# Optimization experiments

Measured on AMD Instinct MI355X. Metric: run time of the kernel, lower is better.

The kernel has to match this reference:

```python
import jax, jax.numpy as jnp
import numpy as np

# Config constants from the module
E = 64    # n_routed_experts
K = 6     # num_experts_per_tok
D = 128   # hidden_size
M = 80    # moe_intermediate_size
MS = 160  # shared expert intermediate = moe_intermediate_size * n_shared_experts
B, S = 64, 256

def _init_w(k, shape, fan_in):
    # kaiming_uniform(a=sqrt(5)) used by nn.Linear / MoEGate: bound = 1/sqrt(fan_in)
    bound = 1.0 / np.sqrt(fan_in)
    return jax.random.uniform(k, shape, jnp.float32, -bound, bound)

def setup_inputs() -> dict:
    key = jax.random.key(0)
    ks = jax.random.split(key, 8)
    return {
        "hidden_states": jax.random.normal(ks[0], (B, S, D), jnp.float32),
        "gate_w": _init_w(ks[1], (E, D), D),        # MoEGate.linear.weight [E, gating_dim]
        "wg": _init_w(ks[2], (E, D, M), D),          # stacked expert gate_proj (transposed)
        "wu": _init_w(ks[3], (E, D, M), D),          # stacked expert up_proj
        "wd": _init_w(ks[4], (E, M, D), M),          # stacked expert down_proj
        "swg": _init_w(ks[5], (D, MS), D),           # shared expert gate_proj
        "swu": _init_w(ks[6], (D, MS), D),           # shared expert up_proj
        "swd": _init_w(ks[7], (MS, D), MS),          # shared expert down_proj
    }

def reference(hidden_states, gate_w, wg, wu, wd, swg, swu, swd):
    orig_shape = hidden_states.shape
    x = hidden_states.reshape(-1, D)                       # [T, D] flat tokens
    T = x.shape[0]
    # --- MoEGate ('all_agent' mode): softmax scoring + top-k + renorm ---
    scores = jax.nn.softmax(x @ gate_w.T, axis=-1)          # [T, E]
    topk_w, topk_idx = jax.lax.top_k(scores, K)             # [T, K]
    topk_w = topk_w / (jnp.sum(topk_w, axis=-1, keepdims=True) + 1e-20)
    # Scatter top-k weights into dense per-expert combine weights [T, E]
    cw = jnp.zeros_like(scores).at[jnp.arange(T)[:, None], topk_idx].add(topk_w)
    # --- Routed experts: SiLU-gated MLP per expert, combined by cw ---
    g = jax.nn.silu(jnp.einsum('td,edm->tem', x, wg)) * jnp.einsum('td,edm->tem', x, wu)
    y = jnp.einsum('tem,emd,te->td', g, wd, cw)             # down-proj + weighted combine
    # --- Shared experts ---
    shared = (jax.nn.silu(x @ swg) * (x @ swu)) @ swd       # [T, D]
    return (y + shared).reshape(orig_shape)
```

## Files before the change

### kernel.cpp

```cpp
#include <hip/hip_runtime.h>
#include <hip/hip_bf16.h>
#include <math.h>


typedef unsigned short ushort_t;
typedef __attribute__((ext_vector_type(8))) short bf16x8;
typedef __attribute__((ext_vector_type(4))) float f32x4;

#define EALL  66

#define OFF_TOPKI 16384
#define OFF_WORK  409600
#define OFF_TOPKW 802816
#define OFF_PERM  1196032
#define OFF_PERMW 1589248
#define OFF_POS2  1982464
#define OFF_YPERM 2375680
#define OFF_YSH   27541504
#define OFF_WGT   31735808
#define OFF_WUT   33087488
#define OFF_WDP   34439168
#define OFF_XB    36061184
#define OFF_HIST  40255488
#define OFF_BOFF  40321024
#define NEED_FAST 40386560
#define FOFF_YBUF 2375680
#define FOFF_WGT  10764288
#define FOFF_WUT  12115968
#define FOFF_WDP  13467648
#define FOFF_XB   15089664
#define FOFF_HIST 19283968
#define FOFF_BOFF 19349504

__device__ __forceinline__ float bf2f(ushort_t u) {
    unsigned int x = ((unsigned int)u) << 16;
    float f; __builtin_memcpy(&f, &x, 4); return f;
}
__device__ __forceinline__ ushort_t f2bf(float f) {
    unsigned int x; __builtin_memcpy(&x, &f, 4);
    unsigned int r = (x + 0x7fffu + ((x >> 16) & 1u)) >> 16;
    return (ushort_t)r;
}
__device__ __forceinline__ float ldin(const void* p, int i, int f32m) {
    return f32m ? ((const float*)p)[i] : bf2f(((const ushort_t*)p)[i]);
}
__device__ __forceinline__ int detect_f32m(const ushort_t* gw) {
    int lane = threadIdx.x & 63;
    int cnt = 0;
    #pragma unroll
    for (int j = 0; j < 4; ++j) {
        ushort_t u = gw[lane * 4 + j];
        if (((u >> 7) & 0xFF) >= 0x7C) cnt++;
    }
    #pragma unroll
    for (int off = 32; off; off >>= 1) cnt += __shfl_xor(cnt, off);
    return (cnt >= 8) ? 1 : 0;
}
__device__ __forceinline__ void gl16(void* l, const void* g) {
    __builtin_amdgcn_global_load_lds(
        (const __attribute__((address_space(1))) void*)g,
        (__attribute__((address_space(3))) void*)l, 16, 0, 0);
}

__global__ __launch_bounds__(1024) void k_pg(const void* x, const void* gw,
        const void* wg, const void* wu, const void* wd,
        const void* swg, const void* swu, const void* swd,
        ushort_t* wgT, ushort_t* wuT, ushort_t* wdP,
        ushort_t* xB, int* topk_i, float* topk_w, int* histPart) {
    __shared__ __align__(16) char smem[41984];
    int tid = threadIdx.x, bid = blockIdx.x;
    int f32m = detect_f32m((const ushort_t*)gw);

    if (bid < 3 * EALL) {
        float* lds = (float*)smem;
        int mat = bid / EALL, e = bid % EALL;
        if (mat < 2) {
            const void* src  = (mat == 0) ? wg  : wu;
            const void* ssrc = (mat == 0) ? swg : swu;
            for (int i = tid; i < 10240; i += 1024) {
                int d = i / 80, m = i % 80;
                float v = (e < 64) ? ldin(src, e * 10240 + i, f32m)
                                   : ldin(ssrc, d * 160 + (e - 64) * 80 + m, f32m);
                lds[d * 81 + m] = v;
            }
            __syncthreads();
            ushort_t* dst = ((mat == 0) ? wgT : wuT) + e * 10240;
            for (int o = tid; o < 10240; o += 1024) {
                int m = o >> 7, d = o & 127;
                dst[o] = f2bf(lds[d * 81 + m]);
            }
        } else {
            for (int i = tid; i < 10240; i += 1024) {
                float v = (e < 64) ? ldin(wd, e * 10240 + i, f32m)
                                   : ldin(swd, (e - 64) * 10240 + i, f32m);
                int m = i >> 7, d = i & 127;
                lds[m * 129 + d] = v;
            }
            __syncthreads();
            ushort_t* dst = wdP + e * 12288;
            for (int o = tid; o < 12288; o += 1024) {
                int d = o / 96, m = o % 96;
                dst[o] = (m < 80) ? f2bf(lds[m * 129 + d]) : (ushort_t)0;
            }
        }
        return;
    }

    float* gwl  = (float*)smem;
    float (*xl)[128] = (float(*)[128])(smem + 33280);
    int*   histL = (int*)(smem + 41472);
    int b = bid - 3 * EALL;
    for (int i = tid; i < 8192; i += 1024)
        gwl[(i >> 7) * 130 + (i & 127)] = ldin(gw, i, f32m);
    if (tid < 64) histL[tid] = 0;
    __syncthreads();
    int wv = tid >> 6, lane = tid & 63;
    for (int q = 0; q < 4; ++q) {
        int t = b * 64 + wv * 4 + q;
        float xv0, xv1;
        if (f32m) {
            float2 v = ((const float2*)((const float*)x + t * 128))[lane];
            xv0 = v.x; xv1 = v.y;
        } else {
            unsigned int pr = *(const unsigned int*)((const ushort_t*)x + t * 128 + lane * 2);
            xv0 = bf2f((ushort_t)(pr & 0xffffu));
            xv1 = bf2f((ushort_t)(pr >> 16));
        }
        float2 xw; xw.x = xv0; xw.y = xv1;
        *(float2*)&xl[wv][lane * 2] = xw;
        unsigned int packed = (unsigned int)f2bf(xv0) | ((unsigned int)f2bf(xv1) << 16);
        *(unsigned int*)(xB + t * 128 + lane * 2) = packed;
        float acc = 0.f;
        #pragma unroll
        for (int d2 = 0; d2 < 64; ++d2) {
            float2 xv = *(const float2*)&xl[wv][d2 * 2];
            float2 gv = *(const float2*)&gwl[lane * 130 + d2 * 2];
            acc = fmaf(xv.x, gv.x, acc);
            acc = fmaf(xv.y, gv.y, acc);
        }
        float mx = acc;
        #pragma unroll
        for (int off = 32; off; off >>= 1) mx = fmaxf(mx, __shfl_xor(mx, off));
        float p = expf(acc - mx);
        float sm = p;
        #pragma unroll
        for (int off = 32; off; off >>= 1) sm += __shfl_xor(sm, off);
        float sc = p / sm;
        float cur = sc;
        float wk6[6]; int ik[6];
        #pragma unroll
        for (int k = 0; k < 6; ++k) {
            float bv = cur; int bi = lane;
            #pragma unroll
            for (int off = 1; off < 64; off <<= 1) {
                float ov = __shfl_xor(bv, off); int oi = __shfl_xor(bi, off);
                if (ov > bv || (ov == bv && oi < bi)) { bv = ov; bi = oi; }
            }
            wk6[k] = bv; ik[k] = bi;
            if (lane == bi) cur = -INFINITY;
        }
        if (lane == 0) {
            float den = wk6[0] + wk6[1] + wk6[2] + wk6[3] + wk6[4] + wk6[5] + 1e-20f;
            #pragma unroll
            for (int k = 0; k < 6; ++k) {
                topk_i[t * 6 + k] = ik[k];
                topk_w[t * 6 + k] = wk6[k] / den;
                atomicAdd(&histL[ik[k]], 1);
            }
        }
    }
    __syncthreads();
    if (tid < 64) histPart[tid * 256 + b] = histL[tid];
}

__global__ __launch_bounds__(256) void k_scan(int* Wi, const int* histPart,
        int* boffG, int* wk) {
    __shared__ int hl[16384];
    __shared__ int cntL[64], exclL[64], chxL[65];
    int tid = threadIdx.x, lane = tid & 63, wv = tid >> 6;
    for (int j = tid; j < 16384; j += 256) hl[j] = histPart[j];
    __syncthreads();
    for (int ei = 0; ei < 16; ++ei) {
        int e = wv * 16 + ei;
        int carry = 0;
        for (int r = 0; r < 4; ++r) {
            int v = hl[e * 256 + r * 64 + lane];
            int incl = v;
            #pragma unroll
            for (int off = 1; off < 64; off <<= 1) {
                int ts = __shfl_up(incl, off);
                if (lane >= off) incl += ts;
            }
            hl[e * 256 + r * 64 + lane] = carry + incl - v;
            carry += __shfl(incl, 63);
        }
        if (lane == 0) cntL[e] = carry;
    }
    __syncthreads();
    if (tid == 0) {
        int s = 0, cs = 0;
        for (int e = 0; e < 64; ++e) {
            exclL[e] = s; s += cntL[e];
            chxL[e] = cs; cs += (cntL[e] + 127) >> 7;
        }
        chxL[64] = cs;
        Wi[128] = s;
        Wi[193] = cs + 256;
    }
    __syncthreads();
    if (tid < 64) { Wi[tid] = cntL[tid]; Wi[64 + tid] = exclL[tid]; }
    for (int j = tid; j < 16384; j += 256) boffG[j] = hl[j] + exclL[j >> 8];
    wk[tid] = (64 << 16) | tid;
    if (tid < 64) {
        int e = tid, nc = (cntL[e] + 127) >> 7, bb = chxL[e];
        for (int c = 0; c < nc; ++c) wk[256 + bb + c] = (e << 16) | c;
    }
}

__global__ __launch_bounds__(256) void k_scatter(const int* topk_i, const float* topk_w,
        const int* boffG, int* perm, float* permw, int* pos2) {
    __shared__ int lcur[64];
    int tid = threadIdx.x, b = blockIdx.x;
    if (tid < 64) lcur[tid] = boffG[tid * 256 + b];
    __syncthreads();
    for (int i = tid; i < 384; i += 256) {
        int g = b * 384 + i;
        int e = topk_i[g];
        float w = topk_w[g];
        int p = atomicAdd(&lcur[e], 1);
        perm[p]  = b * 64 + i / 6;
        permw[p] = w;
        pos2[g]  = p;
    }
}

template<int FAST>
__global__ __launch_bounds__(256) void k_expert(const ushort_t* x, const ushort_t* wgT,
        const ushort_t* wuT, const ushort_t* wdP, const int* Wi, const int* wk,
        const int* perm, const float* permw, ushort_t* yperm, ushort_t* ysh, float* ybuf) {
    __shared__ __align__(16) char hl[32768];
    __shared__ __align__(16) char bufA[20480];
    __shared__ __align__(16) char bufB[20480];

    if (blockIdx.x >= Wi[193]) return;
    int entry = wk[blockIdx.x];
    int e = entry >> 16, c = entry & 0xffff;
    int tid = threadIdx.x, lid = tid & 63, wv = tid >> 6;
    int kg  = (lid >> 4) * 16;
    int kq8 = (lid >> 4) * 8;

    if (e < 64) {
        int n = Wi[e], base = Wi[64 + e];
        int nrows = n - c * 128; if (nrows > 128) nrows = 128;

        {
            const ushort_t* gS = wgT + e * 10240;
            const ushort_t* uS = wuT + e * 10240;
            #pragma unroll
            for (int i = 0; i < 5; ++i) {
                int s = wv * 320 + i * 64 + lid;
                int row = s >> 4, sc = (s & 15) ^ (row & 7);
                gl16(bufA + wv * 5120 + i * 1024, gS + row * 128 + sc * 8);
                gl16(bufB + wv * 5120 + i * 1024, uS + row * 128 + sc * 8);
            }
        }
        bf16x8 a[2][4];
        #pragma unroll
        for (int tr = 0; tr < 2; ++tr) {
            int arow = wv * 32 + tr * 16 + (lid & 15);
            int r = (arow < nrows) ? arow : (nrows - 1);
            int t = perm[base + c * 128 + r];
            #pragma unroll
            for (int k = 0; k < 4; ++k)
                a[tr][k] = *(const bf16x8*)(x + t * 128 + k * 32 + kq8);
        }
        __syncthreads();

        #pragma unroll
        for (int mi = 0; mi < 5; ++mi) {
            int brow = mi * 16 + (lid & 15);
            int bro = brow * 256, bsw = (brow & 7) << 4;
            f32x4 ag[2], au[2];
            #pragma unroll
            for (int tr = 0; tr < 2; ++tr) {
                ag[tr] = (f32x4){0.f, 0.f, 0.f, 0.f};
                au[tr] = (f32x4){0.f, 0.f, 0.f, 0.f};
            }
            #pragma unroll
            for (int k = 0; k < 4; ++k) {
                int bo = bro + (((k * 64) + kg) ^ bsw);
                bf16x8 bg = *(const bf16x8*)(bufA + bo);
                bf16x8 bu = *(const bf16x8*)(bufB + bo);
                #pragma unroll
                for (int tr = 0; tr < 2; ++tr) {
                    ag[tr] = __builtin_amdgcn_mfma_f32_16x16x32_bf16(a[tr][k], bg, ag[tr], 0, 0, 0);
                    au[tr] = __builtin_amdgcn_mfma_f32_16x16x32_bf16(a[tr][k], bu, au[tr], 0, 0, 0);
                }
            }
            #pragma unroll
            for (int tr = 0; tr < 2; ++tr) {
                #pragma unroll
                for (int rg = 0; rg < 4; ++rg) {
                    float g = ag[tr][rg], uu2 = au[tr][rg];
                    float h = (g / (1.f + __expf(-g))) * uu2;
                    int row = wv * 32 + tr * 16 + (lid >> 4) * 4 + rg;
                    int cb = (mi * 16 + (lid & 15)) * 2;
                    *(ushort_t*)(hl + row * 256 + (cb ^ ((row & 7) << 4))) = f2bf(h);
                }
            }
        }
        {
            int r = wv * 32 + (lid >> 1), ch = 10 + (lid & 1);
            uint4 z = {0u, 0u, 0u, 0u};
            *(uint4*)(hl + r * 256 + ((ch * 16) ^ ((r & 7) << 4))) = z;
        }
        __syncthreads();

        {
            const ushort_t* dS = wdP + e * 12288;
            #pragma unroll
            for (int i = 0; i < 4; ++i) {
                int s = wv * 256 + i * 64 + lid;
                int r = s >> 4, sc = (s & 15) ^ (r & 7);
                int off = (sc < 12) ? sc * 8 : 0;
                gl16(bufA + wv * 4096 + i * 1024, dS + r * 96 + off);
                gl16(bufB + wv * 4096 + i * 1024, dS + (64 + r) * 96 + off);
            }
        }
        __syncthreads();

        bf16x8 bfr[2][3];
        #pragma unroll
        for (int tf = 0; tf < 2; ++tf) {
            int brow = wv * 32 + tf * 16 + (lid & 15);
            #pragma unroll
            for (int k = 0; k < 3; ++k)
                bfr[tf][k] = *(const bf16x8*)(hl + brow * 256 + (((k * 64) + kg) ^ ((brow & 7) << 4)));
        }
        f32x4 acc[8][2];
        #pragma unroll
        for (int dt = 0; dt < 8; ++dt) {
            acc[dt][0] = (f32x4){0.f, 0.f, 0.f, 0.f};
            acc[dt][1] = (f32x4){0.f, 0.f, 0.f, 0.f};
        }
        #pragma unroll
        for (int dt = 0; dt < 8; ++dt) {
            int r = (dt & 3) * 16 + (lid & 15);
            const char* wb = (dt < 4) ? bufA : bufB;
            bf16x8 ad[3];
            #pragma unroll
            for (int k = 0; k < 3; ++k)
                ad[k] = *(const bf16x8*)(wb + r * 256 + (((k * 64) + kg) ^ ((r & 7) << 4)));
            #pragma unroll
            for (int tf = 0; tf < 2; ++tf) {
                f32x4 cc = acc[dt][tf];
                #pragma unroll
                for (int k = 0; k < 3; ++k)
                    cc = __builtin_amdgcn_mfma_f32_16x16x32_bf16(ad[k], bfr[tf][k], cc, 0, 0, 0);
                acc[dt][tf] = cc;
            }
        }

        #pragma unroll
        for (int tf = 0; tf < 2; ++tf) {
            int rloc = wv * 32 + tf * 16 + (lid & 15);
            int rc = (rloc < nrows) ? rloc : (nrows - 1);
            float w = FAST ? permw[base + c * 128 + rc] : 0.f;
            #pragma unroll
            for (int dt = 0; dt < 8; ++dt) {
                if (FAST) {
                    int cb = (dt * 16 + (lid >> 4) * 4) * 2;
                    ushort_t o[4];
                    #pragma unroll
                    for (int rg = 0; rg < 4; ++rg) o[rg] = f2bf(acc[dt][tf][rg] * w);
                    *(uint2*)(hl + rloc * 256 + (cb ^ ((rloc & 7) << 4))) = *(const uint2*)o;
                } else {
                    if (rloc < nrows) {
                        int t = perm[base + c * 128 + rloc];
                        float w2 = permw[base + c * 128 + rloc];
                        int d0 = dt * 16 + (lid >> 4) * 4;
                        #pragma unroll
                        for (int rg = 0; rg < 4; ++rg)
                            atomicAdd(&ybuf[t * 128 + d0 + rg], acc[dt][tf][rg] * w2);
                    }
                }
            }
        }
        if (FAST) {
            #pragma unroll
            for (int ps = 0; ps < 8; ++ps) {
                int row = wv * 32 + ps * 4 + (lid >> 4);
                int cb = (lid & 15) * 16;
                uint4 v = *(const uint4*)(hl + row * 256 + (cb ^ ((row & 7) << 4)));
                if (row < nrows)
                    *(uint4*)(yperm + (size_t)(base + c * 128 + row) * 128 + (lid & 15) * 8) = v;
            }
        }
    } else {
        bf16x8 a1[4];
        int arow = wv * 16 + (lid & 15);
        int t0 = c * 64 + arow;
        #pragma unroll
        for (int k = 0; k < 4; ++k)
            a1[k] = *(const bf16x8*)(x + t0 * 128 + k * 32 + kq8);

        f32x4 acc[8];
        #pragma unroll
        for (int dt = 0; dt < 8; ++dt) acc[dt] = (f32x4){0.f, 0.f, 0.f, 0.f};

        for (int sub = 0; sub < 2; ++sub) {
            int ee = 64 + sub;
            {
                const ushort_t* gS = wgT + ee * 10240;
                const ushort_t* uS = wuT + ee * 10240;
                #pragma unroll
                for (int i = 0; i < 5; ++i) {
                    int s = wv * 320 + i * 64 + lid;
                    int row = s >> 4, sc = (s & 15) ^ (row & 7);
                    gl16(bufA + wv * 5120 + i * 1024, gS + row * 128 + sc * 8);
                    gl16(bufB + wv * 5120 + i * 1024, uS + row * 128 + sc * 8);
                }
            }
            __syncthreads();
            #pragma unroll
            for (int mi = 0; mi < 5; ++mi) {
                int brow = mi * 16 + (lid & 15);
                int bro = brow * 256, bsw = (brow & 7) << 4;
                f32x4 ag = {0.f, 0.f, 0.f, 0.f};
                f32x4 au = {0.f, 0.f, 0.f, 0.f};
                #pragma unroll
                for (int k = 0; k < 4; ++k) {
                    int bo = bro + (((k * 64) + kg) ^ bsw);
                    bf16x8 bg = *(const bf16x8*)(bufA + bo);
                    bf16x8 bu = *(const bf16x8*)(bufB + bo);
                    ag = __builtin_amdgcn_mfma_f32_16x16x32_bf16(a1[k], bg, ag, 0, 0, 0);
                    au = __builtin_amdgcn_mfma_f32_16x16x32_bf16(a1[k], bu, au, 0, 0, 0);
                }
                #pragma unroll
                for (int rg = 0; rg < 4; ++rg) {
                    float g = ag[rg], uu2 = au[rg];
                    float h = (g / (1.f + __expf(-g))) * uu2;
                    int row = wv * 16 + (lid >> 4) * 4 + rg;
                    int cb = (mi * 16 + (lid & 15)) * 2;
                    *(ushort_t*)(hl + row * 256 + (cb ^ ((row & 7) << 4))) = f2bf(h);
                }
            }
            if (sub == 0 && lid < 32) {
                int r = wv * 16 + (lid >> 1), ch = 10 + (lid & 1);
                uint4 z = {0u, 0u, 0u, 0u};
                *(uint4*)(hl + r * 256 + ((ch * 16) ^ ((r & 7) << 4))) = z;
            }
            __syncthreads();
            {
                const ushort_t* dS = wdP + ee * 12288;
                #pragma unroll
                for (int i = 0; i < 4; ++i) {
                    int s = wv * 256 + i * 64 + lid;
                    int r = s >> 4, sc = (s & 15) ^ (r & 7);
                    int off = (sc < 12) ? sc * 8 : 0;
                    gl16(bufA + wv * 4096 + i * 1024, dS + r * 96 + off);
                    gl16(bufB + wv * 4096 + i * 1024, dS + (64 + r) * 96 + off);
                }
            }
            __syncthreads();
            int brow = wv * 16 + (lid & 15);
            #pragma unroll
            for (int dt = 0; dt < 8; ++dt) {
                int r = (dt & 3) * 16 + (lid & 15);
                const char* wb = (dt < 4) ? bufA : bufB;
                bf16x8 ad[3];
                #pragma unroll
                for (int k = 0; k < 3; ++k)
                    ad[k] = *(const bf16x8*)(wb + r * 256 + (((k * 64) + kg) ^ ((r & 7) << 4)));
                f32x4 cc = acc[dt];
                #pragma unroll
                for (int k = 0; k < 3; ++k) {
                    bf16x8 b = *(const bf16x8*)(hl + brow * 256 + (((k * 64) + kg) ^ ((brow & 7) << 4)));
                    cc = __builtin_amdgcn_mfma_f32_16x16x32_bf16(ad[k], b, cc, 0, 0, 0);
                }
                acc[dt] = cc;
            }
            __syncthreads();
        }

        int rloc = wv * 16 + (lid & 15);
        if (FAST) {
            #pragma unroll
            for (int dt = 0; dt < 8; ++dt) {
                int cb = (dt * 16 + (lid >> 4) * 4) * 2;
                ushort_t o[4];
                #pragma unroll
                for (int rg = 0; rg < 4; ++rg) o[rg] = f2bf(acc[dt][rg]);
                *(uint2*)(hl + rloc * 256 + (cb ^ ((rloc & 7) << 4))) = *(const uint2*)o;
            }
            #pragma unroll
            for (int ps = 0; ps < 4; ++ps) {
                int row = wv * 16 + ps * 4 + (lid >> 4);
                int cb = (lid & 15) * 16;
                uint4 v = *(const uint4*)(hl + row * 256 + (cb ^ ((row & 7) << 4)));
                *(uint4*)(ysh + (size_t)(c * 64 + row) * 128 + (lid & 15) * 8) = v;
            }
        } else {
            int t = c * 64 + rloc;
            #pragma unroll
            for (int dt = 0; dt < 8; ++dt) {
                int d0 = dt * 16 + (lid >> 4) * 4;
                #pragma unroll
                for (int rg = 0; rg < 4; ++rg)
                    atomicAdd(&ybuf[t * 128 + d0 + rg], acc[dt][rg]);
            }
        }
    }
}

__global__ __launch_bounds__(256) void k_final_gather(const ushort_t* yperm,
        const ushort_t* ysh, const int* pos2, void* out, const ushort_t* gwDet) {
    int idx = blockIdx.x * 256 + threadIdx.x;
    int t = idx >> 4, cg = (idx & 15) * 8;
    int f32m = detect_f32m(gwDet);
    float acc[8];
    {
        uint4 v = *(const uint4*)(ysh + (size_t)t * 128 + cg);
        const ushort_t* u = (const ushort_t*)&v;
        #pragma unroll
        for (int j = 0; j < 8; ++j) acc[j] = bf2f(u[j]);
    }
    const int* pp = pos2 + t * 6;
    #pragma unroll
    for (int k = 0; k < 6; ++k) {
        int p = pp[k];
        uint4 v = *(const uint4*)(yperm + (size_t)p * 128 + cg);
        const ushort_t* u = (const ushort_t*)&v;
        #pragma unroll
        for (int j = 0; j < 8; ++j) acc[j] += bf2f(u[j]);
    }
    if (f32m) {
        float4 o0 = {acc[0], acc[1], acc[2], acc[3]};
        float4 o1 = {acc[4], acc[5], acc[6], acc[7]};
        float* op = (float*)out + (size_t)t * 128 + cg;
        *(float4*)op = o0; *(float4*)(op + 4) = o1;
    } else {
        ushort_t o[8];
        #pragma unroll
        for (int j = 0; j < 8; ++j) o[j] = f2bf(acc[j]);
        *(uint4*)((ushort_t*)out + (size_t)t * 128 + cg) = *(const uint4*)o;
    }
}

__global__ __launch_bounds__(256) void k_final_ybuf(const float* ybuf, void* out,
        const ushort_t* gwDet) {
    int i = blockIdx.x * 256 + threadIdx.x;
    int f32m = detect_f32m(gwDet);
    float4 v = ((const float4*)ybuf)[i];
    if (f32m) {
        ((float4*)out)[i] = v;
    } else {
        ushort4 o;
        o.x = f2bf(v.x); o.y = f2bf(v.y); o.z = f2bf(v.z); o.w = f2bf(v.w);
        ((ushort4*)out)[i] = o;
    }
}

extern "C" void kernel_launch(void* const* d_in, const int* in_sizes, int n_in,
                              void* d_out, int out_size, void* d_ws, size_t ws_size,
                              hipStream_t stream) {
    (void)in_sizes; (void)n_in; (void)out_size;
    const void* x   = d_in[0];
    const void* gw  = d_in[1];
    const void* wg  = d_in[2];
    const void* wu  = d_in[3];
    const void* wd  = d_in[4];
    const void* swg = d_in[5];
    const void* swu = d_in[6];
    const void* swd = d_in[7];

    char* ws = (char*)d_ws;
    int fast = (ws_size >= (size_t)NEED_FAST) ? 1 : 0;

    int*      Wi     = (int*)d_ws;
    int*      topk_i = (int*)(ws + OFF_TOPKI);
    int*      wklist = (int*)(ws + OFF_WORK);
    float*    topk_w = (float*)(ws + OFF_TOPKW);
    int*      perm   = (int*)(ws + OFF_PERM);
    float*    permw  = (float*)(ws + OFF_PERMW);
    int*      pos2   = (int*)(ws + OFF_POS2);

    ushort_t* yperm = (ushort_t*)(ws + OFF_YPERM);
    ushort_t* ysh   = (ushort_t*)(ws + OFF_YSH);
    float*    ybuf  = (float*)(ws + FOFF_YBUF);
    ushort_t* wgT   = (ushort_t*)(ws + (fast ? OFF_WGT  : FOFF_WGT));
    ushort_t* wuT   = (ushort_t*)(ws + (fast ? OFF_WUT  : FOFF_WUT));
    ushort_t* wdP   = (ushort_t*)(ws + (fast ? OFF_WDP  : FOFF_WDP));
    ushort_t* xB    = (ushort_t*)(ws + (fast ? OFF_XB   : FOFF_XB));
    int*      histP = (int*)(ws + (fast ? OFF_HIST : FOFF_HIST));
    int*      boffG = (int*)(ws + (fast ? OFF_BOFF : FOFF_BOFF));

    if (!fast) hipMemsetAsync(ybuf, 0, 16384 * 128 * 4, stream);

    k_pg<<<3 * EALL + 256, 1024, 0, stream>>>(x, gw, wg, wu, wd, swg, swu, swd,
                                              wgT, wuT, wdP, xB, topk_i, topk_w, histP);
    k_scan<<<1, 256, 0, stream>>>(Wi, histP, boffG, wklist);
    k_scatter<<<256, 256, 0, stream>>>(topk_i, topk_w, boffG, perm, permw, pos2);
    if (fast) {
        k_expert<1><<<1088, 256, 0, stream>>>(xB, wgT, wuT, wdP, Wi, wklist, perm, permw, yperm, ysh, ybuf);
        k_final_gather<<<1024, 256, 0, stream>>>(yperm, ysh, pos2, d_out, (const ushort_t*)gw);
    } else {
        k_expert<0><<<1088, 256, 0, stream>>>(xB, wgT, wuT, wdP, Wi, wklist, perm, permw, yperm, ysh, ybuf);
        k_final_ybuf<<<2048, 256, 0, stream>>>(ybuf, d_out, (const ushort_t*)gw);
    }
}
```

Before: 92.65 us.

## Fuse scan into scatter, derive expert work in-kernel, shrink expert LDS staging

The single-block scan kernel is merged into the scatter kernel: every scatter block redundantly loads the 64x256 histogram and scans it itself. This removes one launch and the boffG and work-list global round trips. The expert kernel now computes its (expert, chunk) assignment from the per-expert counts with a wave prefix-scan and ballot, so the precomputed work list is no longer needed. Weight staging buffers shrink from 20KB to 8KB each and weights are streamed in smaller chunks with extra barriers, cutting LDS per block to raise occupancy. The cost is redundant scan work in 256 blocks and more synchronisation points inside the expert kernel.

```diff
diff --git a/kernel.cpp b/kernel.cpp
--- a/kernel.cpp
+++ b/kernel.cpp
@@ -173,11 +173,11 @@
     if (tid < 64) histPart[tid * 256 + b] = histL[tid];
 }
 
-__global__ __launch_bounds__(256) void k_scan(int* Wi, const int* histPart,
-        int* boffG, int* wk) {
+__global__ __launch_bounds__(256) void k_scatter(int* Wi, const int* histPart,
+        const int* topk_i, const float* topk_w, int* perm, float* permw, int* pos2) {
     __shared__ int hl[16384];
-    __shared__ int cntL[64], exclL[64], chxL[65];
-    int tid = threadIdx.x, lane = tid & 63, wv = tid >> 6;
+    __shared__ int cntL[64], exclL[64], lcur[64];
+    int tid = threadIdx.x, lane = tid & 63, wv = tid >> 6, b = blockIdx.x;
     for (int j = tid; j < 16384; j += 256) hl[j] = histPart[j];
     __syncthreads();
     for (int ei = 0; ei < 16; ++ei) {
@@ -198,30 +198,12 @@
     }
     __syncthreads();
     if (tid == 0) {
-        int s = 0, cs = 0;
-        for (int e = 0; e < 64; ++e) {
-            exclL[e] = s; s += cntL[e];
-            chxL[e] = cs; cs += (cntL[e] + 127) >> 7;
-        }
-        chxL[64] = cs;
-        Wi[128] = s;
-        Wi[193] = cs + 256;
+        int s = 0;
+        for (int e = 0; e < 64; ++e) { exclL[e] = s; s += cntL[e]; }
     }
     __syncthreads();
-    if (tid < 64) { Wi[tid] = cntL[tid]; Wi[64 + tid] = exclL[tid]; }
-    for (int j = tid; j < 16384; j += 256) boffG[j] = hl[j] + exclL[j >> 8];
-    wk[tid] = (64 << 16) | tid;
-    if (tid < 64) {
-        int e = tid, nc = (cntL[e] + 127) >> 7, bb = chxL[e];
-        for (int c = 0; c < nc; ++c) wk[256 + bb + c] = (e << 16) | c;
-    }
-}
-
-__global__ __launch_bounds__(256) void k_scatter(const int* topk_i, const float* topk_w,
-        const int* boffG, int* perm, float* permw, int* pos2) {
-    __shared__ int lcur[64];
-    int tid = threadIdx.x, b = blockIdx.x;
-    if (tid < 64) lcur[tid] = boffG[tid * 256 + b];
+    if (b == 0 && tid < 64) { Wi[tid] = cntL[tid]; Wi[64 + tid] = exclL[tid]; }
+    if (tid < 64) lcur[tid] = hl[tid * 256 + b] + exclL[tid];
     __syncthreads();
     for (int i = tid; i < 384; i += 256) {
         int g = b * 384 + i;
@@ -236,34 +218,43 @@
 
 template<int FAST>
 __global__ __launch_bounds__(256) void k_expert(const ushort_t* x, const ushort_t* wgT,
-        const ushort_t* wuT, const ushort_t* wdP, const int* Wi, const int* wk,
+        const ushort_t* wuT, const ushort_t* wdP, const int* Wi,
         const int* perm, const float* permw, ushort_t* yperm, ushort_t* ysh, float* ybuf) {
     __shared__ __align__(16) char hl[32768];
-    __shared__ __align__(16) char bufA[20480];
-    __shared__ __align__(16) char bufB[20480];
-
-    if (blockIdx.x >= Wi[193]) return;
-    int entry = wk[blockIdx.x];
-    int e = entry >> 16, c = entry & 0xffff;
+    __shared__ __align__(16) char bufA[8192];
+    __shared__ __align__(16) char bufB[8192];
+
     int tid = threadIdx.x, lid = tid & 63, wv = tid >> 6;
+    int bid = blockIdx.x;
     int kg  = (lid >> 4) * 16;
     int kq8 = (lid >> 4) * 8;
+
+    int e, c;
+    if (bid < 256) {
+        e = 64; c = bid;
+    } else {
+        int cnt_l = Wi[lid];
+        int nc = (cnt_l + 127) >> 7;
+        int incl = nc;
+        #pragma unroll
+        for (int off = 1; off < 64; off <<= 1) {
+            int t2 = __shfl_up(incl, off);
+            if (lid >= off) incl += t2;
+        }
+        int totalR = __shfl(incl, 63);
+        int rb = bid - 256;
+        if (rb >= totalR) return;
+        int epref = incl - nc;
+        unsigned long long m = __ballot(rb >= epref && rb < incl);
+        int src = (int)__builtin_ctzll(m);
+        e = src;
+        c = rb - __shfl(epref, src);
+    }
 
     if (e < 64) {
         int n = Wi[e], base = Wi[64 + e];
         int nrows = n - c * 128; if (nrows > 128) nrows = 128;
 
-        {
-            const ushort_t* gS = wgT + e * 10240;
-            const ushort_t* uS = wuT + e * 10240;
-            #pragma unroll
-            for (int i = 0; i < 5; ++i) {
-                int s = wv * 320 + i * 64 + lid;
-                int row = s >> 4, sc = (s & 15) ^ (row & 7);
-                gl16(bufA + wv * 5120 + i * 1024, gS + row * 128 + sc * 8);
-                gl16(bufB + wv * 5120 + i * 1024, uS + row * 128 + sc * 8);
-            }
-        }
         bf16x8 a[2][4];
         #pragma unroll
         for (int tr = 0; tr < 2; ++tr) {
@@ -274,61 +265,68 @@
             for (int k = 0; k < 4; ++k)
                 a[tr][k] = *(const bf16x8*)(x + t * 128 + k * 32 + kq8);
         }
-        __syncthreads();
-
-        #pragma unroll
-        for (int mi = 0; mi < 5; ++mi) {
-            int brow = mi * 16 + (lid & 15);
-            int bro = brow * 256, bsw = (brow & 7) << 4;
-            f32x4 ag[2], au[2];
-            #pragma unroll
-            for (int tr = 0; tr < 2; ++tr) {
-                ag[tr] = (f32x4){0.f, 0.f, 0.f, 0.f};
-                au[tr] = (f32x4){0.f, 0.f, 0.f, 0.f};
-            }
-            #pragma unroll
-            for (int k = 0; k < 4; ++k) {
-                int bo = bro + (((k * 64) + kg) ^ bsw);
-                bf16x8 bg = *(const bf16x8*)(bufA + bo);
-                bf16x8 bu = *(const bf16x8*)(bufB + bo);
+
+        const ushort_t* gS = wgT + e * 10240;
+        const ushort_t* uS = wuT + e * 10240;
+
+        #pragma unroll
+        for (int g = 0; g < 3; ++g) {
+            int rbase = g * 32;
+            int units = (g == 2) ? 256 : 512;
+            #pragma unroll
+            for (int i = 0; i < 2; ++i) {
+                int s = i * 256 + tid;
+                if (s < units) {
+                    int row = rbase + (s >> 4);
+                    int sc = (s & 15) ^ (row & 7);
+                    gl16(bufA + (size_t)s * 16, gS + row * 128 + sc * 8);
+                    gl16(bufB + (size_t)s * 16, uS + row * 128 + sc * 8);
+                }
+            }
+            __syncthreads();
+            int nmi = (g == 2) ? 1 : 2;
+            for (int m2 = 0; m2 < nmi; ++m2) {
+                int mi = 2 * g + m2;
+                int brow = mi * 16 + (lid & 15);
+                int lro = (brow - rbase) * 256;
+                int bsw = (brow & 7) << 4;
+                f32x4 ag[2], au[2];
                 #pragma unroll
                 for (int tr = 0; tr < 2; ++tr) {
-                    ag[tr] = __builtin_amdgcn_mfma_f32_16x16x32_bf16(a[tr][k], bg, ag[tr], 0, 0, 0);
-                    au[tr] = __builtin_amdgcn_mfma_f32_16x16x32_bf16(a[tr][k], bu, au[tr], 0, 0, 0);
-                }
-            }
-            #pragma unroll
-            for (int tr = 0; tr < 2; ++tr) {
-                #pragma unroll
-                for (int rg = 0; rg < 4; ++rg) {
-                    float g = ag[tr][rg], uu2 = au[tr][rg];
-                    float h = (g / (1.f + __expf(-g))) * uu2;
-                    int row = wv * 32 + tr * 16 + (lid >> 4) * 4 + rg;
-                    int cb = (mi * 16 + (lid & 15)) * 2;
-                    *(ushort_t*)(hl + row * 256 + (cb ^ ((row & 7) << 4))) = f2bf(h);
-                }
-            }
-        }
+                    ag[tr] = (f32x4){0.f, 0.f, 0.f, 0.f};
+                    au[tr] = (f32x4){0.f, 0.f, 0.f, 0.f};
+                }
+                #pragma unroll
+                for (int k = 0; k < 4; ++k) {
+                    int bo = lro + (((k * 64) + kg) ^ bsw);
+                    bf16x8 bg = *(const bf16x8*)(bufA + bo);
+                    bf16x8 bu = *(const bf16x8*)(bufB + bo);
+                    #pragma unroll
+                    for (int tr = 0; tr < 2; ++tr) {
+                        ag[tr] = __builtin_amdgcn_mfma_f32_16x16x32_bf16(a[tr][k], bg, ag[tr], 0, 0, 0);
+                        au[tr] = __builtin_amdgcn_mfma_f32_16x16x32_bf16(a[tr][k], bu, au[tr], 0, 0, 0);
+                    }
+                }
+                #pragma unroll
+                for (int tr = 0; tr < 2; ++tr) {
+                    #pragma unroll
+                    for (int rg = 0; rg < 4; ++rg) {
+                        float gg = ag[tr][rg], uu2 = au[tr][rg];
+                        float h = (gg / (1.f + __expf(-gg))) * uu2;
+                        int row = wv * 32 + tr * 16 + (lid >> 4) * 4 + rg;
+                        int cb = (mi * 16 + (lid & 15)) * 2;
+                        *(ushort_t*)(hl + row * 256 + (cb ^ ((row & 7) << 4))) = f2bf(h);
+                    }
+                }
+            }
+            __syncthreads();
+        }
+
         {
             int r = wv * 32 + (lid >> 1), ch = 10 + (lid & 1);
             uint4 z = {0u, 0u, 0u, 0u};
             *(uint4*)(hl + r * 256 + ((ch * 16) ^ ((r & 7) << 4))) = z;
         }
-        __syncthreads();
-
-        {
-            const ushort_t* dS = wdP + e * 12288;
-            #pragma unroll
-            for (int i = 0; i < 4; ++i) {
-                int s = wv * 256 + i * 64 + lid;
-                int r = s >> 4, sc = (s & 15) ^ (r & 7);
-                int off = (sc < 12) ? sc * 8 : 0;
-                gl16(bufA + wv * 4096 + i * 1024, dS + r * 96 + off);
-                gl16(bufB + wv * 4096 + i * 1024, dS + (64 + r) * 96 + off);
-            }
-        }
-        __syncthreads();
-
         bf16x8 bfr[2][3];
         #pragma unroll
         for (int tf = 0; tf < 2; ++tf) {
@@ -337,28 +335,50 @@
             for (int k = 0; k < 3; ++k)
                 bfr[tf][k] = *(const bf16x8*)(hl + brow * 256 + (((k * 64) + kg) ^ ((brow & 7) << 4)));
         }
+
         f32x4 acc[8][2];
         #pragma unroll
         for (int dt = 0; dt < 8; ++dt) {
             acc[dt][0] = (f32x4){0.f, 0.f, 0.f, 0.f};
             acc[dt][1] = (f32x4){0.f, 0.f, 0.f, 0.f};
         }
-        #pragma unroll
-        for (int dt = 0; dt < 8; ++dt) {
-            int r = (dt & 3) * 16 + (lid & 15);
-            const char* wb = (dt < 4) ? bufA : bufB;
-            bf16x8 ad[3];
-            #pragma unroll
-            for (int k = 0; k < 3; ++k)
-                ad[k] = *(const bf16x8*)(wb + r * 256 + (((k * 64) + kg) ^ ((r & 7) << 4)));
-            #pragma unroll
-            for (int tf = 0; tf < 2; ++tf) {
-                f32x4 cc = acc[dt][tf];
+        const ushort_t* dS = wdP + e * 12288;
+        #pragma unroll
+        for (int h = 0; h < 2; ++h) {
+            #pragma unroll
+            for (int i = 0; i < 2; ++i) {
+                int s = i * 256 + tid;
+                int r = s >> 4, ch = s & 15;
+                int rowA = h * 64 + r;
+                int scA = ch ^ (rowA & 7);
+                int offA = (scA < 12) ? scA * 8 : 0;
+                gl16(bufA + (size_t)s * 16, dS + rowA * 96 + offA);
+                int rowB = rowA + 32;
+                int scB = ch ^ (rowB & 7);
+                int offB = (scB < 12) ? scB * 8 : 0;
+                gl16(bufB + (size_t)s * 16, dS + rowB * 96 + offB);
+            }
+            __syncthreads();
+            #pragma unroll
+            for (int d2 = 0; d2 < 4; ++d2) {
+                int dt = h * 4 + d2;
+                int grow = dt * 16 + (lid & 15);
+                int lr = (d2 & 1) * 16 + (lid & 15);
+                const char* wb = (d2 < 2) ? bufA : bufB;
+                bf16x8 ad[3];
                 #pragma unroll
                 for (int k = 0; k < 3; ++k)
-                    cc = __builtin_amdgcn_mfma_f32_16x16x32_bf16(ad[k], bfr[tf][k], cc, 0, 0, 0);
-                acc[dt][tf] = cc;
-            }
+                    ad[k] = *(const bf16x8*)(wb + lr * 256 + (((k * 64) + kg) ^ ((grow & 7) << 4)));
+                #pragma unroll
+                for (int tf = 0; tf < 2; ++tf) {
+                    f32x4 cc = acc[dt][tf];
+                    #pragma unroll
+                    for (int k = 0; k < 3; ++k)
+                        cc = __builtin_amdgcn_mfma_f32_16x16x32_bf16(ad[k], bfr[tf][k], cc, 0, 0, 0);
+                    acc[dt][tf] = cc;
+                }
+            }
+            __syncthreads();
         }
 
         #pragma unroll
@@ -410,77 +430,99 @@
 
         for (int sub = 0; sub < 2; ++sub) {
             int ee = 64 + sub;
-            {
-                const ushort_t* gS = wgT + ee * 10240;
-                const ushort_t* uS = wuT + ee * 10240;
-                #pragma unroll
-                for (int i = 0; i < 5; ++i) {
-                    int s = wv * 320 + i * 64 + lid;
-                    int row = s >> 4, sc = (s & 15) ^ (row & 7);
-                    gl16(bufA + wv * 5120 + i * 1024, gS + row * 128 + sc * 8);
-                    gl16(bufB + wv * 5120 + i * 1024, uS + row * 128 + sc * 8);
-                }
-            }
-            __syncthreads();
-            #pragma unroll
-            for (int mi = 0; mi < 5; ++mi) {
-                int brow = mi * 16 + (lid & 15);
-                int bro = brow * 256, bsw = (brow & 7) << 4;
-                f32x4 ag = {0.f, 0.f, 0.f, 0.f};
-                f32x4 au = {0.f, 0.f, 0.f, 0.f};
-                #pragma unroll
-                for (int k = 0; k < 4; ++k) {
-                    int bo = bro + (((k * 64) + kg) ^ bsw);
-                    bf16x8 bg = *(const bf16x8*)(bufA + bo);
-                    bf16x8 bu = *(const bf16x8*)(bufB + bo);
-                    ag = __builtin_amdgcn_mfma_f32_16x16x32_bf16(a1[k], bg, ag, 0, 0, 0);
-                    au = __builtin_amdgcn_mfma_f32_16x16x32_bf16(a1[k], bu, au, 0, 0, 0);
-                }
-                #pragma unroll
-                for (int rg = 0; rg < 4; ++rg) {
-                    float g = ag[rg], uu2 = au[rg];
-                    float h = (g / (1.f + __expf(-g))) * uu2;
-                    int row = wv * 16 + (lid >> 4) * 4 + rg;
-                    int cb = (mi * 16 + (lid & 15)) * 2;
-                    *(ushort_t*)(hl + row * 256 + (cb ^ ((row & 7) << 4))) = f2bf(h);
-                }
+            const ushort_t* gS = wgT + ee * 10240;
+            const ushort_t* uS = wuT + ee * 10240;
+
+            #pragma unroll
+            for (int g = 0; g < 3; ++g) {
+                int rbase = g * 32;
+                int units = (g == 2) ? 256 : 512;
+                #pragma unroll
+                for (int i = 0; i < 2; ++i) {
+                    int s = i * 256 + tid;
+                    if (s < units) {
+                        int row = rbase + (s >> 4);
+                        int sc = (s & 15) ^ (row & 7);
+                        gl16(bufA + (size_t)s * 16, gS + row * 128 + sc * 8);
+                        gl16(bufB + (size_t)s * 16, uS + row * 128 + sc * 8);
+                    }
+                }
+                __syncthreads();
+                int nmi = (g == 2) ? 1 : 2;
+                for (int m2 = 0; m2 < nmi; ++m2) {
+                    int mi = 2 * g + m2;
+                    int brow = mi * 16 + (lid & 15);
+                    int lro = (brow - rbase) * 256;
+                    int bsw = (brow & 7) << 4;
+                    f32x4 ag = {0.f, 0.f, 0.f, 0.f};
+                    f32x4 au = {0.f, 0.f, 0.f, 0.f};
+                    #pragma unroll
+                    for (int k = 0; k < 4; ++k) {
+                        int bo = lro + (((k * 64) + kg) ^ bsw);
+                        bf16x8 bg = *(const bf16x8*)(bufA + bo);
+                        bf16x8 bu = *(const bf16x8*)(bufB + bo);
+                        ag = __builtin_amdgcn_mfma_f32_16x16x32_bf16(a1[k], bg, ag, 0, 0, 0);
+                        au = __builtin_amdgcn_mfma_f32_16x16x32_bf16(a1[k], bu, au, 0, 0, 0);
+                    }
+                    #pragma unroll
+                    for (int rg = 0; rg < 4; ++rg) {
+                        float gg = ag[rg], uu2 = au[rg];
+                        float h = (gg / (1.f + __expf(-gg))) * uu2;
+                        int row = wv * 16 + (lid >> 4) * 4 + rg;
+                        int cb = (mi * 16 + (lid & 15)) * 2;
+                        *(ushort_t*)(hl + row * 256 + (cb ^ ((row & 7) << 4))) = f2bf(h);
+                    }
+                }
+                __syncthreads();
             }
             if (sub == 0 && lid < 32) {
                 int r = wv * 16 + (lid >> 1), ch = 10 + (lid & 1);
                 uint4 z = {0u, 0u, 0u, 0u};
                 *(uint4*)(hl + r * 256 + ((ch * 16) ^ ((r & 7) << 4))) = z;
             }
-            __syncthreads();
+            bf16x8 bfr1[3];
             {
-                const ushort_t* dS = wdP + ee * 12288;
-                #pragma unroll
-                for (int i = 0; i < 4; ++i) {
-                    int s = wv * 256 + i * 64 + lid;
-                    int r = s >> 4, sc = (s & 15) ^ (r & 7);
-                    int off = (sc < 12) ? sc * 8 : 0;
-                    gl16(bufA + wv * 4096 + i * 1024, dS + r * 96 + off);
-                    gl16(bufB + wv * 4096 + i * 1024, dS + (64 + r) * 96 + off);
-                }
-            }
-            __syncthreads();
-            int brow = wv * 16 + (lid & 15);
-            #pragma unroll
-            for (int dt = 0; dt < 8; ++dt) {
-                int r = (dt & 3) * 16 + (lid & 15);
-                const char* wb = (dt < 4) ? bufA : bufB;
-                bf16x8 ad[3];
+                int brow = wv * 16 + (lid & 15);
                 #pragma unroll
                 for (int k = 0; k < 3; ++k)
-                    ad[k] = *(const bf16x8*)(wb + r * 256 + (((k * 64) + kg) ^ ((r & 7) << 4)));
-                f32x4 cc = acc[dt];
-                #pragma unroll
-                for (int k = 0; k < 3; ++k) {
-                    bf16x8 b = *(const bf16x8*)(hl + brow * 256 + (((k * 64) + kg) ^ ((brow & 7) << 4)));
-                    cc = __builtin_amdgcn_mfma_f32_16x16x32_bf16(ad[k], b, cc, 0, 0, 0);
-                }
-                acc[dt] = cc;
-            }
-            __syncthreads();
+                    bfr1[k] = *(const bf16x8*)(hl + brow * 256 + (((k * 64) + kg) ^ ((brow & 7) << 4)));
+            }
+
+            const ushort_t* dS = wdP + ee * 12288;
+            #pragma unroll
+            for (int h = 0; h < 2; ++h) {
+                #pragma unroll
+                for (int i = 0; i < 2; ++i) {
+                    int s = i * 256 + tid;
+                    int r = s >> 4, ch = s & 15;
+                    int rowA = h * 64 + r;
+                    int scA = ch ^ (rowA & 7);
+                    int offA = (scA < 12) ? scA * 8 : 0;
+                    gl16(bufA + (size_t)s * 16, dS + rowA * 96 + offA);
+                    int rowB = rowA + 32;
+                    int scB = ch ^ (rowB & 7);
+                    int offB = (scB < 12) ? scB * 8 : 0;
+                    gl16(bufB + (size_t)s * 16, dS + rowB * 96 + offB);
+                }
+                __syncthreads();
+                #pragma unroll
+                for (int d2 = 0; d2 < 4; ++d2) {
+                    int dt = h * 4 + d2;
+                    int grow = dt * 16 + (lid & 15);
+                    int lr = (d2 & 1) * 16 + (lid & 15);
+                    const char* wb = (d2 < 2) ? bufA : bufB;
+                    bf16x8 ad[3];
+                    #pragma unroll
+                    for (int k = 0; k < 3; ++k)
+                        ad[k] = *(const bf16x8*)(wb + lr * 256 + (((k * 64) + kg) ^ ((grow & 7) << 4)));
+                    f32x4 cc = acc[dt];
+                    #pragma unroll
+                    for (int k = 0; k < 3; ++k)
+                        cc = __builtin_amdgcn_mfma_f32_16x16x32_bf16(ad[k], bfr1[k], cc, 0, 0, 0);
+                    acc[dt] = cc;
+                }
+                __syncthreads();
+            }
         }
 
         int rloc = wv * 16 + (lid & 15);
@@ -579,7 +621,6 @@
 
     int*      Wi     = (int*)d_ws;
     int*      topk_i = (int*)(ws + OFF_TOPKI);
-    int*      wklist = (int*)(ws + OFF_WORK);
     float*    topk_w = (float*)(ws + OFF_TOPKW);
     int*      perm   = (int*)(ws + OFF_PERM);
     float*    permw  = (float*)(ws + OFF_PERMW);
@@ -593,19 +634,17 @@
     ushort_t* wdP   = (ushort_t*)(ws + (fast ? OFF_WDP  : FOFF_WDP));
     ushort_t* xB    = (ushort_t*)(ws + (fast ? OFF_XB   : FOFF_XB));
     int*      histP = (int*)(ws + (fast ? OFF_HIST : FOFF_HIST));
-    int*      boffG = (int*)(ws + (fast ? OFF_BOFF : FOFF_BOFF));
 
     if (!fast) hipMemsetAsync(ybuf, 0, 16384 * 128 * 4, stream);
 
     k_pg<<<3 * EALL + 256, 1024, 0, stream>>>(x, gw, wg, wu, wd, swg, swu, swd,
                                               wgT, wuT, wdP, xB, topk_i, topk_w, histP);
-    k_scan<<<1, 256, 0, stream>>>(Wi, histP, boffG, wklist);
-    k_scatter<<<256, 256, 0, stream>>>(topk_i, topk_w, boffG, perm, permw, pos2);
+    k_scatter<<<256, 256, 0, stream>>>(Wi, histP, topk_i, topk_w, perm, permw, pos2);
     if (fast) {
-        k_expert<1><<<1088, 256, 0, stream>>>(xB, wgT, wuT, wdP, Wi, wklist, perm, permw, yperm, ysh, ybuf);
+        k_expert<1><<<1088, 256, 0, stream>>>(xB, wgT, wuT, wdP, Wi, perm, permw, yperm, ysh, ybuf);
         k_final_gather<<<1024, 256, 0, stream>>>(yperm, ysh, pos2, d_out, (const ushort_t*)gw);
     } else {
-        k_expert<0><<<1088, 256, 0, stream>>>(xB, wgT, wuT, wdP, Wi, wklist, perm, permw, yperm, ysh, ybuf);
+        k_expert<0><<<1088, 256, 0, stream>>>(xB, wgT, wuT, wdP, Wi, perm, permw, yperm, ysh, ybuf);
         k_final_ybuf<<<2048, 256, 0, stream>>>(ybuf, d_out, (const ushort_t*)gw);
     }
 }
```

Result: no change. 93.53 us (+0.9%).
